# Performance work log

Measured on AMD Instinct MI355X. Metric: run time of the kernel, lower is better.

Reference implementation:

```python
import jax, jax.numpy as jnp
import numpy as np

EPS = 1e-12  # torch F.normalize default eps


def l2_normalize_c(x):
    # F.normalize over channel dim (dim=1): x / max(||x||_2, eps)
    nrm = jnp.sqrt(jnp.sum(x * x, axis=1, keepdims=True))
    return x / jnp.maximum(nrm, EPS)


def resize_bilinear_ac(x, H, W):
    # bilinear, align_corners=True (matches torch F.interpolate)
    n, c, h, w = x.shape
    ys = jnp.linspace(0.0, h - 1.0, H)
    xs = jnp.linspace(0.0, w - 1.0, W)
    y0 = jnp.floor(ys).astype(jnp.int32)
    y1 = jnp.minimum(y0 + 1, h - 1)
    wy = (ys - y0.astype(ys.dtype))[:, None]          # [H,1]
    x0 = jnp.floor(xs).astype(jnp.int32)
    x1 = jnp.minimum(x0 + 1, w - 1)
    wx = xs - x0.astype(xs.dtype)                      # [W]
    rows = x[:, :, y0, :] * (1.0 - wy) + x[:, :, y1, :] * wy   # [n,c,H,w]
    return rows[:, :, :, x0] * (1.0 - wx) + rows[:, :, :, x1] * wx  # [n,c,H,W]


def unfold_3x3_d2(x):
    # nn.Unfold(kernel=3, dilation=2, padding=2, stride=1) viewed as [n,c,9,h,w]
    n, c, h, w = x.shape
    xp = jnp.pad(x, ((0, 0), (0, 0), (2, 2), (2, 2)))
    return jnp.stack(
        [xp[:, :, dy:dy + h, dx:dx + w] for dy in (0, 2, 4) for dx in (0, 2, 4)],
        axis=2,
    )  # [n,c,9,h,w], kernel index row-major (ky*3+kx) matching torch unfold


def setup_inputs() -> dict:
    key = jax.random.key(0)
    k1, k2, k3, k4, k5 = jax.random.split(key, 5)
    return {
        "c1": jax.random.normal(k1, (4, 256, 128, 128), dtype=jnp.float32),
        "c2": jax.random.normal(k2, (4, 512, 64, 64), dtype=jnp.float32),
        "out": jax.random.normal(k3, (4, 256, 64, 64), dtype=jnp.float32),
        "w_refine": jax.random.normal(k4, (32, 256), dtype=jnp.float32) * 0.05,
        "w_refine2": jax.random.normal(k5, (32, 512), dtype=jnp.float32) * 0.05,
    }


def reference(c1, c2, out, w_refine, w_refine2):
    n, _, h, w = c1.shape
    # 1x1 conv (no bias) + L2 normalize over channels
    q = l2_normalize_c(jnp.einsum("nchw,kc->nkhw", c1, w_refine))       # [n,32,h,w]
    c2u = resize_bilinear_ac(c2, h, w)
    kft = l2_normalize_c(jnp.einsum("nchw,kc->nkhw", c2u, w_refine2))    # [n,32,h,w]
    kpat = unfold_3x3_d2(kft)                                            # [n,32,9,h,w]
    energy = jnp.einsum("nchw,nckhw->nkhw", q, kpat)                     # [n,9,h,w]
    att = jax.nn.softmax(energy, axis=1)
    outu = resize_bilinear_ac(out, h, w)                                 # [n,C,h,w]
    vpat = unfold_3x3_d2(outu)                                           # [n,C,9,h,w]
    return jnp.einsum("nkhw,nckhw->nchw", att, vpat)
```

## Files before the change

kernel.cpp:

```cpp
#include <hip/hip_runtime.h>
#include <hip/hip_bf16.h>


typedef float f32x4 __attribute__((ext_vector_type(4)));
typedef float f32x2 __attribute__((ext_vector_type(2)));

#define SCL (63.0f / 127.0f)

__global__ __launch_bounds__(1024) void k_kfs(const float* __restrict__ c2,
                                              const float* __restrict__ wr2,
                                              float* __restrict__ kfs) {
    __shared__ float red[8 * 32 * 66];
    int b = blockIdx.x;
    int n = b >> 6;
    int pblk = (b & 63) * 64;
    int t = threadIdx.x;
    int lane = t & 63;
    int w = t >> 6;
    int cg = __builtin_amdgcn_readfirstlane(w & 7);
    int og = __builtin_amdgcn_readfirstlane(w >> 3);

    const float* src = c2 + ((size_t)n * 512 + cg * 64) * 4096 + pblk + lane;
    const float* wp  = wr2 + (og * 16) * 512 + cg * 64;

    float acc[16];
#pragma unroll
    for (int o = 0; o < 16; ++o) acc[o] = 0.f;
#pragma unroll 4
    for (int c = 0; c < 64; ++c) {
        float v = src[(size_t)c * 4096];
#pragma unroll
        for (int o = 0; o < 16; ++o)
            acc[o] = fmaf(v, wp[o * 512 + c], acc[o]);
    }
#pragma unroll
    for (int o = 0; o < 16; ++o)
        red[(cg * 32 + og * 16 + o) * 66 + lane] = acc[o];
    __syncthreads();

    if (t < 512) {
        int px = t & 63, seg = t >> 6;
        float v[4];
#pragma unroll
        for (int j = 0; j < 4; ++j) {
            float r = 0.f;
#pragma unroll
            for (int g = 0; g < 8; ++g) r += red[(g * 32 + seg * 4 + j) * 66 + px];
            v[j] = r;
        }
        f32x4 o4 = { v[0], v[1], v[2], v[3] };
        *(f32x4*)(kfs + ((size_t)n * 4096 + pblk + px) * 32 + seg * 4) = o4;
    }
}

__global__ __launch_bounds__(256) void k_upnorm(const float* __restrict__ kfs,
                                                float* __restrict__ kft) {
    int g = blockIdx.x * 256 + threadIdx.x;
    int p = g >> 2, qt = g & 3;
    int n = p >> 14;
    int rem = p & 16383;
    int y = rem >> 7, x = rem & 127;
    float syf = SCL * (float)y; int y0 = (int)syf; float fy = syf - (float)y0;
    int y1 = min(y0 + 1, 63);
    float sxf = SCL * (float)x; int x0 = (int)sxf; float fx = sxf - (float)x0;
    int x1 = min(x0 + 1, 63);
    size_t base = (size_t)n * 4096 * 32 + qt * 8;
    const f32x4* p00 = (const f32x4*)(kfs + base + ((size_t)(y0 * 64 + x0)) * 32);
    const f32x4* p01 = (const f32x4*)(kfs + base + ((size_t)(y0 * 64 + x1)) * 32);
    const f32x4* p10 = (const f32x4*)(kfs + base + ((size_t)(y1 * 64 + x0)) * 32);
    const f32x4* p11 = (const f32x4*)(kfs + base + ((size_t)(y1 * 64 + x1)) * 32);
    float w00 = (1.f-fy)*(1.f-fx), w01 = (1.f-fy)*fx, w10 = fy*(1.f-fx), w11 = fy*fx;
    float v[8]; float s = 0.f;
#pragma unroll
    for (int j = 0; j < 2; ++j) {
        f32x4 a = p00[j], b = p01[j], c = p10[j], d = p11[j];
#pragma unroll
        for (int tt = 0; tt < 4; ++tt) {
            float r = a[tt]*w00 + b[tt]*w01 + c[tt]*w10 + d[tt]*w11;
            v[4*j + tt] = r;
            s = fmaf(r, r, s);
        }
    }
    s += __shfl_xor(s, 1, 4);
    s += __shfl_xor(s, 2, 4);
    float inv = 1.0f / fmaxf(sqrtf(s), 1e-12f);
    f32x4* dst = (f32x4*)(kft + (size_t)p * 32 + qt * 8);
#pragma unroll
    for (int j = 0; j < 2; ++j) {
        f32x4 t = { v[4*j]*inv, v[4*j+1]*inv, v[4*j+2]*inv, v[4*j+3]*inv };
        dst[j] = t;
    }
}

__global__ __launch_bounds__(512) void k_fqa(const float* __restrict__ c1,
                                             const float* __restrict__ wr,
                                             const float* __restrict__ kft,
                                             const float* __restrict__ outp,
                                             float* __restrict__ res) {
    __shared__ float smem[16640];
    const int WOFF = 4224, TOFF = 6400;
    int b = blockIdx.x;
    int n = b >> 7;
    int y = b & 127;
    int pblk = y * 128;
    int t = threadIdx.x;
    int lane = t & 63;
    int w = t >> 6;
    int cg = __builtin_amdgcn_readfirstlane(w & 3);
    int og = __builtin_amdgcn_readfirstlane(w >> 2);

    {
        const float* src = c1 + ((size_t)n * 256 + cg * 64) * 16384 + pblk + lane * 2;
        const float* wp  = wr + (og * 16) * 256 + cg * 64;
        float acc0[16], acc1[16];
#pragma unroll
        for (int o = 0; o < 16; ++o) { acc0[o] = 0.f; acc1[o] = 0.f; }
#pragma unroll 4
        for (int c = 0; c < 64; ++c) {
            f32x2 v = *(const f32x2*)(src + (size_t)c * 16384);
#pragma unroll
            for (int o = 0; o < 16; ++o) {
                float wv = wp[o * 256 + c];
                acc0[o] = fmaf(v[0], wv, acc0[o]);
                acc1[o] = fmaf(v[1], wv, acc1[o]);
            }
        }
#pragma unroll
        for (int o = 0; o < 16; ++o) {
            f32x2 pr = { acc0[o], acc1[o] };
            *(f32x2*)&smem[(cg * 32 + og * 16 + o) * 130 + lane * 2] = pr;
        }
    }
    __syncthreads();

    float v16[16];
    {
        int px = t & 127, half = (t >> 7) & 1;
        if (t < 256) {
#pragma unroll
            for (int o = 0; o < 16; ++o) {
                v16[o] = smem[(0 * 32 + half * 16 + o) * 130 + px]
                       + smem[(1 * 32 + half * 16 + o) * 130 + px]
                       + smem[(2 * 32 + half * 16 + o) * 130 + px]
                       + smem[(3 * 32 + half * 16 + o) * 130 + px];
            }
        }
    }
    __syncthreads();
    if (t < 256) {
        int px = t & 127, half = (t >> 7) & 1;
#pragma unroll
        for (int o = 0; o < 16; ++o) smem[px * 33 + half * 16 + o] = v16[o];
    }
    __syncthreads();

    {
        int px = t >> 2, qt = t & 3;
        int x = px;
        int ybase2 = min((int)(SCL * (float)max(y - 2, 0)), 60);
        int xbase2 = min((int)(SCL * (float)max(x - 2, 0)), 60);

        float qv[8];
#pragma unroll
        for (int j = 0; j < 8; ++j) qv[j] = smem[px * 33 + qt * 8 + j];
        float qs = 0.f;
#pragma unroll
        for (int j = 0; j < 8; ++j) qs = fmaf(qv[j], qv[j], qs);

        float d[9];
#pragma unroll
        for (int ky = 0; ky < 3; ++ky) {
            int ny = y + 2 * ky - 2;
            bool rowOK = (ny >= 0) && (ny < 128);
#pragma unroll
            for (int kx = 0; kx < 3; ++kx) {
                int nx = x + 2 * kx - 2;
                float acc = 0.f;
                if (rowOK && nx >= 0 && nx < 128) {
                    const f32x4* kp = (const f32x4*)(kft + ((size_t)n * 16384 + ny * 128 + nx) * 32 + qt * 8);
                    f32x4 a = kp[0], b2 = kp[1];
                    acc = fmaf(a[0],  qv[0], acc); acc = fmaf(a[1],  qv[1], acc);
                    acc = fmaf(a[2],  qv[2], acc); acc = fmaf(a[3],  qv[3], acc);
                    acc = fmaf(b2[0], qv[4], acc); acc = fmaf(b2[1], qv[5], acc);
                    acc = fmaf(b2[2], qv[6], acc); acc = fmaf(b2[3], qv[7], acc);
                }
                d[ky * 3 + kx] = acc;
            }
        }
        qs += __shfl_xor(qs, 1, 4); qs += __shfl_xor(qs, 2, 4);
#pragma unroll
        for (int k = 0; k < 9; ++k) {
            d[k] += __shfl_xor(d[k], 1, 4);
            d[k] += __shfl_xor(d[k], 2, 4);
        }
        float qinv = 1.0f / fmaxf(sqrtf(qs), 1e-12f);

        float e[9];
        float m = d[0] * qinv;
#pragma unroll
        for (int k = 0; k < 9; ++k) { e[k] = d[k] * qinv; if (k) m = fmaxf(m, e[k]); }
        float ssum = 0.f;
#pragma unroll
        for (int k = 0; k < 9; ++k) { e[k] = __expf(e[k] - m); ssum += e[k]; }
        float rinv = 1.0f / ssum;

        float* wp = smem + WOFF + px * 17;
#pragma unroll
        for (int i = 0; i < 16; ++i) wp[i] = 0.f;
#pragma unroll
        for (int ky = 0; ky < 3; ++ky) {
            int ny = y + 2 * ky - 2;
            if (ny < 0 || ny > 127) continue;
            float syf = SCL * (float)ny; int iy0 = (int)syf; float fy = syf - (float)iy0;
            int iy1 = min(iy0 + 1, 63);
            int r0 = (iy0 - ybase2) * 4, r1 = (iy1 - ybase2) * 4;
#pragma unroll
            for (int kx = 0; kx < 3; ++kx) {
                int nx = x + 2 * kx - 2;
                if (nx < 0 || nx > 127) continue;
                float sxf = SCL * (float)nx; int ix0 = (int)sxf; float fx = sxf - (float)ix0;
                int ix1 = min(ix0 + 1, 63);
                float a = e[ky * 3 + kx] * rinv;
                wp[r0 + (ix0 - xbase2)] += a * (1.f - fy) * (1.f - fx);
                wp[r0 + (ix1 - xbase2)] += a * (1.f - fy) * fx;
                wp[r1 + (ix0 - xbase2)] += a * fy * (1.f - fx);
                wp[r1 + (ix1 - xbase2)] += a * fy * fx;
            }
        }
    }
    __syncthreads();

    int px2 = t & 63, cq = t >> 6;
    int x0 = px2 * 2, x1 = x0 + 1;
    int xb0 = min((int)(SCL * (float)max(x0 - 2, 0)), 60);
    int xb1 = min((int)(SCL * (float)max(x1 - 2, 0)), 60);
    bool sh = (xb1 != xb0);
    float wA[16], wB[16];
#pragma unroll
    for (int i = 0; i < 16; ++i) {
        wA[i] = smem[WOFF + x0 * 17 + i];
        wB[i] = smem[WOFF + x1 * 17 + i];
    }
    int ybase = min((int)(SCL * (float)max(y - 2, 0)), 60);

    const float* ob = outp + ((size_t)n * 256) * 4096 + ybase * 64;
    float* rb = res + ((size_t)n * 256) * 16384 + y * 128 + x0;

#pragma unroll 1
    for (int batch = 0; batch < 8; ++batch) {
        __syncthreads();
#pragma unroll
        for (int k = 0; k < 4; ++k) {
            int u = t + 512 * k;
            int cl = u >> 6, seg = u & 63;
            f32x4 v = *(const f32x4*)(ob + (size_t)(batch * 32 + cl) * 4096 + seg * 4);
            *(f32x4*)&smem[TOFF + cl * 260 + seg * 4] = v;
        }
        __syncthreads();
#pragma unroll
        for (int cc = 0; cc < 4; ++cc) {
            int c = cq * 4 + cc;
            const float* tp = &smem[TOFF + c * 260 + xb0];
            float a0 = 0.f, a1 = 0.f;
#pragma unroll
            for (int r = 0; r < 4; ++r) {
                float c0 = tp[r * 64 + 0];
                float c1 = tp[r * 64 + 1];
                float c2 = tp[r * 64 + 2];
                float c3 = tp[r * 64 + 3];
                float c4 = tp[r * 64 + 4];
                a0 = fmaf(wA[r*4+0], c0, a0);
                a0 = fmaf(wA[r*4+1], c1, a0);
                a0 = fmaf(wA[r*4+2], c2, a0);
                a0 = fmaf(wA[r*4+3], c3, a0);
                float s0 = sh ? c1 : c0;
                float s1 = sh ? c2 : c1;
                float s2 = sh ? c3 : c2;
                float s3 = sh ? c4 : c3;
                a1 = fmaf(wB[r*4+0], s0, a1);
                a1 = fmaf(wB[r*4+1], s1, a1);
                a1 = fmaf(wB[r*4+2], s2, a1);
                a1 = fmaf(wB[r*4+3], s3, a1);
            }
            f32x2 st = { a0, a1 };
            *(f32x2*)(rb + (size_t)(batch * 32 + c) * 16384) = st;
        }
    }
}

extern "C" void kernel_launch(void* const* d_in, const int* in_sizes, int n_in,
                              void* d_out, int out_size, void* d_ws, size_t ws_size,
                              hipStream_t stream) {
    const float* c1   = (const float*)d_in[0];
    const float* c2   = (const float*)d_in[1];
    const float* outp = (const float*)d_in[2];
    const float* wr   = (const float*)d_in[3];
    const float* wr2  = (const float*)d_in[4];
    float* res = (float*)d_out;

    float* kfs_ws = (float*)d_ws;
    float* kft_ws = (float*)((char*)d_ws + 2097152);

    hipLaunchKernelGGL(k_kfs,    dim3(256),  dim3(1024), 0, stream, c2, wr2, kfs_ws);
    hipLaunchKernelGGL(k_upnorm, dim3(1024), dim3(256),  0, stream, kfs_ws, kft_ws);
    hipLaunchKernelGGL(k_fqa,    dim3(512),  dim3(512),  0, stream, c1, wr, kft_ws, outp, res);
}
```

Measured before the change: 77.55 us.

## Split fused query-attention kernel into weight kernel and channel-split aggregation kernel

The single fused kernel, which computed the query projection, attention softmax and value aggregation for one image row per block, is split in two. The first kernel handles half a row per block (1024 blocks) and writes the per-pixel 16 interpolation-folded weights to a global workspace. The second kernel reads those weights back and aggregates over the value tensor with blocks split by row and channel quarter (2048 blocks of 256 threads). This raises parallelism and occupancy and shrinks per-block shared memory. The cost is an extra launch and a global write and read of the weight buffer, and in the first kernel only half the threads do the attention stage.

```diff
diff --git a/kernel.cpp b/kernel.cpp
--- a/kernel.cpp
+++ b/kernel.cpp
@@ -92,17 +92,17 @@
     }
 }
 
-__global__ __launch_bounds__(512) void k_fqa(const float* __restrict__ c1,
+__global__ __launch_bounds__(512) void k_fq2(const float* __restrict__ c1,
                                              const float* __restrict__ wr,
                                              const float* __restrict__ kft,
-                                             const float* __restrict__ outp,
-                                             float* __restrict__ res) {
-    __shared__ float smem[16640];
-    const int WOFF = 4224, TOFF = 6400;
+                                             float* __restrict__ wbuf) {
+    __shared__ float smem[8448];
+    const int WOFF = 2112;
     int b = blockIdx.x;
-    int n = b >> 7;
-    int y = b & 127;
-    int pblk = y * 128;
+    int n = b >> 8;
+    int pblk = (b & 255) * 64;
+    int y = pblk >> 7;
+    int xh = pblk & 127;
     int t = threadIdx.x;
     int lane = t & 63;
     int w = t >> 6;
@@ -110,53 +110,47 @@
     int og = __builtin_amdgcn_readfirstlane(w >> 2);
 
     {
-        const float* src = c1 + ((size_t)n * 256 + cg * 64) * 16384 + pblk + lane * 2;
+        const float* src = c1 + ((size_t)n * 256 + cg * 64) * 16384 + pblk + lane;
         const float* wp  = wr + (og * 16) * 256 + cg * 64;
-        float acc0[16], acc1[16];
-#pragma unroll
-        for (int o = 0; o < 16; ++o) { acc0[o] = 0.f; acc1[o] = 0.f; }
+        float acc[16];
+#pragma unroll
+        for (int o = 0; o < 16; ++o) acc[o] = 0.f;
 #pragma unroll 4
         for (int c = 0; c < 64; ++c) {
-            f32x2 v = *(const f32x2*)(src + (size_t)c * 16384);
-#pragma unroll
-            for (int o = 0; o < 16; ++o) {
-                float wv = wp[o * 256 + c];
-                acc0[o] = fmaf(v[0], wv, acc0[o]);
-                acc1[o] = fmaf(v[1], wv, acc1[o]);
+            float v = src[(size_t)c * 16384];
+#pragma unroll
+            for (int o = 0; o < 16; ++o)
+                acc[o] = fmaf(v, wp[o * 256 + c], acc[o]);
+        }
+#pragma unroll
+        for (int o = 0; o < 16; ++o)
+            smem[(cg * 32 + og * 16 + o) * 66 + lane] = acc[o];
+    }
+    __syncthreads();
+
+    float v8[8];
+    {
+        int px = t & 63, kg = (t >> 6) & 3;
+        if (t < 256) {
+#pragma unroll
+            for (int o = 0; o < 8; ++o) {
+                int k = kg * 8 + o;
+                v8[o] = smem[(0 * 32 + k) * 66 + px] + smem[(1 * 32 + k) * 66 + px]
+                      + smem[(2 * 32 + k) * 66 + px] + smem[(3 * 32 + k) * 66 + px];
             }
         }
-#pragma unroll
-        for (int o = 0; o < 16; ++o) {
-            f32x2 pr = { acc0[o], acc1[o] };
-            *(f32x2*)&smem[(cg * 32 + og * 16 + o) * 130 + lane * 2] = pr;
-        }
-    }
-    __syncthreads();
-
-    float v16[16];
-    {
-        int px = t & 127, half = (t >> 7) & 1;
-        if (t < 256) {
-#pragma unroll
-            for (int o = 0; o < 16; ++o) {
-                v16[o] = smem[(0 * 32 + half * 16 + o) * 130 + px]
-                       + smem[(1 * 32 + half * 16 + o) * 130 + px]
-                       + smem[(2 * 32 + half * 16 + o) * 130 + px]
-                       + smem[(3 * 32 + half * 16 + o) * 130 + px];
-            }
-        }
     }
     __syncthreads();
     if (t < 256) {
-        int px = t & 127, half = (t >> 7) & 1;
-#pragma unroll
-        for (int o = 0; o < 16; ++o) smem[px * 33 + half * 16 + o] = v16[o];
-    }
-    __syncthreads();
-
-    {
+        int px = t & 63, kg = (t >> 6) & 3;
+#pragma unroll
+        for (int o = 0; o < 8; ++o) smem[px * 33 + kg * 8 + o] = v8[o];
+    }
+    __syncthreads();
+
+    if (t < 256) {
         int px = t >> 2, qt = t & 3;
-        int x = px;
+        int x = xh + px;
         int ybase2 = min((int)(SCL * (float)max(y - 2, 0)), 60);
         int xbase2 = min((int)(SCL * (float)max(x - 2, 0)), 60);
 
@@ -230,7 +224,38 @@
     }
     __syncthreads();
 
+    {
+        int pg = n * 16384 + pblk;
+#pragma unroll
+        for (int r = 0; r < 2; ++r) {
+            int u = t + 512 * r;
+            int i = u >> 6, pxs = u & 63;
+            wbuf[i * 65536 + pg + pxs] = smem[WOFF + pxs * 17 + i];
+        }
+    }
+}
+
+__global__ __launch_bounds__(256) void k_agg2(const float* __restrict__ wbuf,
+                                              const float* __restrict__ outp,
+                                              float* __restrict__ res) {
+    __shared__ float wlds[128 * 17];
+    __shared__ float tile[8 * 260];
+    int b = blockIdx.x;
+    int cg = b & 3, y = (b >> 2) & 127, n = b >> 9;
+    int t = threadIdx.x;
     int px2 = t & 63, cq = t >> 6;
+
+    int ybase = min((int)(SCL * (float)max(y - 2, 0)), 60);
+    int pix = n * 16384 + y * 128;
+
+#pragma unroll
+    for (int k = 0; k < 8; ++k) {
+        int u = t + 256 * k;
+        int i = u >> 7, xx = u & 127;
+        wlds[xx * 17 + i] = wbuf[i * 65536 + pix + xx];
+    }
+    __syncthreads();
+
     int x0 = px2 * 2, x1 = x0 + 1;
     int xb0 = min((int)(SCL * (float)max(x0 - 2, 0)), 60);
     int xb1 = min((int)(SCL * (float)max(x1 - 2, 0)), 60);
@@ -238,29 +263,28 @@
     float wA[16], wB[16];
 #pragma unroll
     for (int i = 0; i < 16; ++i) {
-        wA[i] = smem[WOFF + x0 * 17 + i];
-        wB[i] = smem[WOFF + x1 * 17 + i];
-    }
-    int ybase = min((int)(SCL * (float)max(y - 2, 0)), 60);
-
-    const float* ob = outp + ((size_t)n * 256) * 4096 + ybase * 64;
-    float* rb = res + ((size_t)n * 256) * 16384 + y * 128 + x0;
+        wA[i] = wlds[x0 * 17 + i];
+        wB[i] = wlds[x1 * 17 + i];
+    }
+
+    const float* ob = outp + ((size_t)n * 256 + cg * 64) * 4096 + ybase * 64;
+    float* rb = res + ((size_t)n * 256 + cg * 64) * 16384 + y * 128 + x0;
 
 #pragma unroll 1
     for (int batch = 0; batch < 8; ++batch) {
         __syncthreads();
 #pragma unroll
-        for (int k = 0; k < 4; ++k) {
-            int u = t + 512 * k;
+        for (int k = 0; k < 2; ++k) {
+            int u = t + 256 * k;
             int cl = u >> 6, seg = u & 63;
-            f32x4 v = *(const f32x4*)(ob + (size_t)(batch * 32 + cl) * 4096 + seg * 4);
-            *(f32x4*)&smem[TOFF + cl * 260 + seg * 4] = v;
+            f32x4 v = *(const f32x4*)(ob + (size_t)(batch * 8 + cl) * 4096 + seg * 4);
+            *(f32x4*)&tile[cl * 260 + seg * 4] = v;
         }
         __syncthreads();
 #pragma unroll
-        for (int cc = 0; cc < 4; ++cc) {
-            int c = cq * 4 + cc;
-            const float* tp = &smem[TOFF + c * 260 + xb0];
+        for (int cc = 0; cc < 2; ++cc) {
+            int c = cq * 2 + cc;
+            const float* tp = &tile[c * 260 + xb0];
             float a0 = 0.f, a1 = 0.f;
 #pragma unroll
             for (int r = 0; r < 4; ++r) {
@@ -283,7 +307,7 @@
                 a1 = fmaf(wB[r*4+3], s3, a1);
             }
             f32x2 st = { a0, a1 };
-            *(f32x2*)(rb + (size_t)(batch * 32 + c) * 16384) = st;
+            *(f32x2*)(rb + (size_t)(batch * 8 + c) * 16384) = st;
         }
     }
 }
@@ -300,8 +324,10 @@
 
     float* kfs_ws = (float*)d_ws;
     float* kft_ws = (float*)((char*)d_ws + 2097152);
+    float* w_ws   = (float*)((char*)d_ws + 2097152 + 8388608);
 
     hipLaunchKernelGGL(k_kfs,    dim3(256),  dim3(1024), 0, stream, c2, wr2, kfs_ws);
     hipLaunchKernelGGL(k_upnorm, dim3(1024), dim3(256),  0, stream, kfs_ws, kft_ws);
-    hipLaunchKernelGGL(k_fqa,    dim3(512),  dim3(512),  0, stream, c1, wr, kft_ws, outp, res);
-}
+    hipLaunchKernelGGL(k_fq2,    dim3(1024), dim3(512),  0, stream, c1, wr, kft_ws, w_ws);
+    hipLaunchKernelGGL(k_agg2,   dim3(2048), dim3(256),  0, stream, w_ws, outp, res);
+}
```

After: 81.19 us. 4.7% more time.

## Split fused attention kernel into weight stage and separate aggregation kernel

Applied to the files above, without the earlier changes.

The fused kernel is split. One kernel computes the per-pixel 16-tap combined attention/bilinear weights and writes them to a workspace buffer. A new aggregation kernel launched with 2048 blocks applies them to the low-resolution values, reading directly from global memory instead of staging them in LDS batches. The c1 projection loop is also software-pipelined with prefetched loads four channels ahead. This trades an extra weight round-trip through memory and one more launch for much higher parallelism in the aggregation phase and fewer barriers.

```diff
diff --git a/kernel.cpp b/kernel.cpp
--- a/kernel.cpp
+++ b/kernel.cpp
@@ -92,13 +92,12 @@
     }
 }
 
-__global__ __launch_bounds__(512) void k_fqa(const float* __restrict__ c1,
+__global__ __launch_bounds__(512) void k_fq3(const float* __restrict__ c1,
                                              const float* __restrict__ wr,
                                              const float* __restrict__ kft,
-                                             const float* __restrict__ outp,
-                                             float* __restrict__ res) {
+                                             float* __restrict__ wbuf) {
     __shared__ float smem[16640];
-    const int WOFF = 4224, TOFF = 6400;
+    const int WOFF = 4224;
     int b = blockIdx.x;
     int n = b >> 7;
     int y = b & 127;
@@ -115,14 +114,30 @@
         float acc0[16], acc1[16];
 #pragma unroll
         for (int o = 0; o < 16; ++o) { acc0[o] = 0.f; acc1[o] = 0.f; }
-#pragma unroll 4
-        for (int c = 0; c < 64; ++c) {
-            f32x2 v = *(const f32x2*)(src + (size_t)c * 16384);
+        f32x2 n0 = *(const f32x2*)(src + (size_t)0 * 16384);
+        f32x2 n1 = *(const f32x2*)(src + (size_t)1 * 16384);
+        f32x2 n2 = *(const f32x2*)(src + (size_t)2 * 16384);
+        f32x2 n3 = *(const f32x2*)(src + (size_t)3 * 16384);
+#pragma unroll
+        for (int cb = 0; cb < 16; ++cb) {
+            f32x2 u0 = n0, u1 = n1, u2 = n2, u3 = n3;
+            if (cb < 15) {
+                const float* s2 = src + (size_t)(cb * 4 + 4) * 16384;
+                n0 = *(const f32x2*)(s2 + (size_t)0 * 16384);
+                n1 = *(const f32x2*)(s2 + (size_t)1 * 16384);
+                n2 = *(const f32x2*)(s2 + (size_t)2 * 16384);
+                n3 = *(const f32x2*)(s2 + (size_t)3 * 16384);
+            }
 #pragma unroll
             for (int o = 0; o < 16; ++o) {
-                float wv = wp[o * 256 + c];
-                acc0[o] = fmaf(v[0], wv, acc0[o]);
-                acc1[o] = fmaf(v[1], wv, acc1[o]);
+                float w0 = wp[o * 256 + cb * 4 + 0];
+                float w1 = wp[o * 256 + cb * 4 + 1];
+                float w2 = wp[o * 256 + cb * 4 + 2];
+                float w3 = wp[o * 256 + cb * 4 + 3];
+                acc0[o] = fmaf(u0[0], w0, acc0[o]); acc1[o] = fmaf(u0[1], w0, acc1[o]);
+                acc0[o] = fmaf(u1[0], w1, acc0[o]); acc1[o] = fmaf(u1[1], w1, acc1[o]);
+                acc0[o] = fmaf(u2[0], w2, acc0[o]); acc1[o] = fmaf(u2[1], w2, acc1[o]);
+                acc0[o] = fmaf(u3[0], w3, acc0[o]); acc1[o] = fmaf(u3[1], w3, acc1[o]);
             }
         }
 #pragma unroll
@@ -230,61 +245,76 @@
     }
     __syncthreads();
 
+    int sx = t & 127, i0 = t >> 7;
+    int pg = n * 16384 + y * 128 + sx;
+#pragma unroll
+    for (int r = 0; r < 4; ++r) {
+        int i = r * 4 + i0;
+        wbuf[i * 65536 + pg] = smem[WOFF + sx * 17 + i];
+    }
+}
+
+__global__ __launch_bounds__(256) void k_agg3(const float* __restrict__ wbuf,
+                                              const float* __restrict__ outp,
+                                              float* __restrict__ res) {
+    __shared__ float wlds[128 * 17];
+    int b = blockIdx.x;
+    int cg = b & 3, y = (b >> 2) & 127, n = b >> 9;
+    int t = threadIdx.x;
     int px2 = t & 63, cq = t >> 6;
+
+    int ybase = min((int)(SCL * (float)max(y - 2, 0)), 60);
+    int pix = n * 16384 + y * 128;
+
+#pragma unroll
+    for (int k = 0; k < 8; ++k) {
+        int u = t + 256 * k;
+        int i = u >> 7, xx = u & 127;
+        wlds[xx * 17 + i] = wbuf[i * 65536 + pix + xx];
+    }
+    __syncthreads();
+
     int x0 = px2 * 2, x1 = x0 + 1;
     int xb0 = min((int)(SCL * (float)max(x0 - 2, 0)), 60);
     int xb1 = min((int)(SCL * (float)max(x1 - 2, 0)), 60);
     bool sh = (xb1 != xb0);
+    int j4 = sh ? 4 : 3;
     float wA[16], wB[16];
 #pragma unroll
     for (int i = 0; i < 16; ++i) {
-        wA[i] = smem[WOFF + x0 * 17 + i];
-        wB[i] = smem[WOFF + x1 * 17 + i];
-    }
-    int ybase = min((int)(SCL * (float)max(y - 2, 0)), 60);
-
-    const float* ob = outp + ((size_t)n * 256) * 4096 + ybase * 64;
-    float* rb = res + ((size_t)n * 256) * 16384 + y * 128 + x0;
-
-#pragma unroll 1
-    for (int batch = 0; batch < 8; ++batch) {
-        __syncthreads();
-#pragma unroll
-        for (int k = 0; k < 4; ++k) {
-            int u = t + 512 * k;
-            int cl = u >> 6, seg = u & 63;
-            f32x4 v = *(const f32x4*)(ob + (size_t)(batch * 32 + cl) * 4096 + seg * 4);
-            *(f32x4*)&smem[TOFF + cl * 260 + seg * 4] = v;
-        }
-        __syncthreads();
-#pragma unroll
-        for (int cc = 0; cc < 4; ++cc) {
-            int c = cq * 4 + cc;
-            const float* tp = &smem[TOFF + c * 260 + xb0];
-            float a0 = 0.f, a1 = 0.f;
-#pragma unroll
-            for (int r = 0; r < 4; ++r) {
-                float c0 = tp[r * 64 + 0];
-                float c1 = tp[r * 64 + 1];
-                float c2 = tp[r * 64 + 2];
-                float c3 = tp[r * 64 + 3];
-                float c4 = tp[r * 64 + 4];
-                a0 = fmaf(wA[r*4+0], c0, a0);
-                a0 = fmaf(wA[r*4+1], c1, a0);
-                a0 = fmaf(wA[r*4+2], c2, a0);
-                a0 = fmaf(wA[r*4+3], c3, a0);
-                float s0 = sh ? c1 : c0;
-                float s1 = sh ? c2 : c1;
-                float s2 = sh ? c3 : c2;
-                float s3 = sh ? c4 : c3;
-                a1 = fmaf(wB[r*4+0], s0, a1);
-                a1 = fmaf(wB[r*4+1], s1, a1);
-                a1 = fmaf(wB[r*4+2], s2, a1);
-                a1 = fmaf(wB[r*4+3], s3, a1);
-            }
-            f32x2 st = { a0, a1 };
-            *(f32x2*)(rb + (size_t)(batch * 32 + c) * 16384) = st;
-        }
+        wA[i] = wlds[x0 * 17 + i];
+        wB[i] = wlds[x1 * 17 + i];
+    }
+
+    const float* ob = outp + ((size_t)n * 256 + cg * 64 + cq * 16) * 4096 + ybase * 64 + xb0;
+    float* rb = res + ((size_t)n * 256 + cg * 64 + cq * 16) * 16384 + y * 128 + x0;
+
+#pragma unroll 2
+    for (int i = 0; i < 16; ++i) {
+        const float* tp = ob + (size_t)i * 4096;
+        float a0 = 0.f, a1 = 0.f;
+#pragma unroll
+        for (int r = 0; r < 4; ++r) {
+            float c0 = tp[r * 64 + 0];
+            float c1 = tp[r * 64 + 1];
+            float c2 = tp[r * 64 + 2];
+            float c3 = tp[r * 64 + 3];
+            float c4 = tp[r * 64 + j4];
+            a0 = fmaf(wA[r*4+0], c0, a0);
+            a0 = fmaf(wA[r*4+1], c1, a0);
+            a0 = fmaf(wA[r*4+2], c2, a0);
+            a0 = fmaf(wA[r*4+3], c3, a0);
+            float s0 = sh ? c1 : c0;
+            float s1 = sh ? c2 : c1;
+            float s2 = sh ? c3 : c2;
+            float s3 = sh ? c4 : c3;
+            a1 = fmaf(wB[r*4+0], s0, a1);
+            a1 = fmaf(wB[r*4+1], s1, a1);
+            a1 = fmaf(wB[r*4+2], s2, a1);
+            a1 = fmaf(wB[r*4+3], s3, a1);
+        }
+        f32x2 st = { a0, a1 };
+        *(f32x2*)(rb + (size_t)i * 16384) = st;
     }
 }
 
@@ -300,8 +330,10 @@
 
     float* kfs_ws = (float*)d_ws;
     float* kft_ws = (float*)((char*)d_ws + 2097152);
+    float* w_ws   = (float*)((char*)d_ws + 2097152 + 8388608);
 
     hipLaunchKernelGGL(k_kfs,    dim3(256),  dim3(1024), 0, stream, c2, wr2, kfs_ws);
     hipLaunchKernelGGL(k_upnorm, dim3(1024), dim3(256),  0, stream, kfs_ws, kft_ws);
-    hipLaunchKernelGGL(k_fqa,    dim3(512),  dim3(512),  0, stream, c1, wr, kft_ws, outp, res);
-}
+    hipLaunchKernelGGL(k_fq3,    dim3(512),  dim3(512),  0, stream, c1, wr, kft_ws, w_ws);
+    hipLaunchKernelGGL(k_agg3,   dim3(2048), dim3(256),  0, stream, w_ws, outp, res);
+}
```

Result: slower. 79.73 us (+2.8%).
